# Performance work log

Hardware: AMD Instinct MI355X
Metric: run time of the kernel (lower is better)

The kernel has to match this reference:

```python
import jax, jax.numpy as jnp
import numpy as np

B, N, D, FF, L = 32, 1000, 128, 512, 6
EPS = 1e-5  # InstanceNorm1d default eps


def _inorm(x, g, b):
    # InstanceNorm1d on [B, d, N] == normalize over sequence dim N per channel (biased var)
    m = jnp.mean(x, axis=1, keepdims=True)
    v = jnp.var(x, axis=1, keepdims=True)
    return (x - m) / jnp.sqrt(v + EPS) * g + b


def setup_inputs() -> dict:
    key = jax.random.key(0)
    ks = jax.random.split(key, 10)
    s = 0.05
    data = jax.random.normal(ks[0], (B, N, 2), dtype=jnp.float32)
    # negative pairwise distances (module calls it negative_dist)
    dist = -jax.random.uniform(ks[1], (B, N, N), dtype=jnp.float32)
    log_scale = jnp.ones((1,), dtype=jnp.float32)
    We = jax.random.normal(ks[2], (D, 2), dtype=jnp.float32) * s
    be = jnp.zeros((D,), dtype=jnp.float32)
    Wq = jax.random.normal(ks[3], (L, D, D), dtype=jnp.float32) * s
    Wk = jax.random.normal(ks[4], (L, D, D), dtype=jnp.float32) * s
    Wv = jax.random.normal(ks[5], (L, D, D), dtype=jnp.float32) * s
    g1 = jnp.ones((L, D), dtype=jnp.float32)
    b1 = jnp.zeros((L, D), dtype=jnp.float32)
    W1 = jax.random.normal(ks[6], (L, FF, D), dtype=jnp.float32) * s
    bw1 = jnp.zeros((L, FF), dtype=jnp.float32)
    W2 = jax.random.normal(ks[7], (L, D, FF), dtype=jnp.float32) * s
    bw2 = jnp.zeros((L, D), dtype=jnp.float32)
    g2 = jnp.ones((L, D), dtype=jnp.float32)
    b2 = jnp.zeros((L, D), dtype=jnp.float32)
    alpha = jnp.ones((L,), dtype=jnp.float32)  # AFT_dist_alpha per layer
    return dict(data=data, dist=dist, log_scale=log_scale, We=We, be=be,
                Wq=Wq, Wk=Wk, Wv=Wv, g1=g1, b1=b1, W1=W1, bw1=bw1,
                W2=W2, bw2=bw2, g2=g2, b2=b2, alpha=alpha)


def reference(data, dist, log_scale, We, be, Wq, Wk, Wv, g1, b1, W1, bw1, W2, bw2, g2, b2, alpha):
    x = data @ We.T + be  # [B,N,D]
    for i in range(L):
        q = x @ Wq[i].T
        k = x @ Wk[i].T
        v = x @ Wv[i].T
        A = jnp.exp(log_scale[0] * alpha[i] * dist)  # [B,N,N]
        ek = jnp.exp(k)
        bias = jnp.einsum('bnm,bmd->bnd', A, ek * v)
        denom = jnp.einsum('bnm,bmd->bnd', A, ek)
        out = jax.nn.sigmoid(q) * (bias / denom)
        x1 = _inorm(x + out, g1[i], b1[i])
        h = jax.nn.relu(x1 @ W1[i].T + bw1[i]) @ W2[i].T + bw2[i]
        x = _inorm(x1 + h, g2[i], b2[i])
    return x
```

## Files before the change

### kernel.cpp

```cpp
#include <hip/hip_runtime.h>
#include <hip/hip_bf16.h>

typedef __attribute__((ext_vector_type(4))) float f32x4;
typedef __attribute__((ext_vector_type(8))) short bf16x8;
typedef __attribute__((ext_vector_type(4))) short s16x4;

#define LCOUNT 6

static __device__ __forceinline__ unsigned short f2b(float f){
  __hip_bfloat16 h = __float2bfloat16(f);
  return __builtin_bit_cast(unsigned short, h);
}
static __device__ __forceinline__ float b2f(unsigned short u){
  unsigned int x = ((unsigned int)u) << 16;
  return __builtin_bit_cast(float, x);
}
static __device__ __forceinline__ void gl16(const void* g, void* l){
  __builtin_amdgcn_global_load_lds(
      (const __attribute__((address_space(1))) void*)g,
      (__attribute__((address_space(3))) void*)l, 16, 0, 0);
}
static __device__ __forceinline__ f32x4 mfma16(bf16x8 a, bf16x8 b, f32x4 c){
  return __builtin_amdgcn_mfma_f32_16x16x32_bf16(a, b, c, 0, 0, 0);
}

__global__ void k_cvt5(const float* __restrict__ Wq, const float* __restrict__ Wk,
                       const float* __restrict__ Wv, const float* __restrict__ W1,
                       const float* __restrict__ W2,
                       unsigned short* __restrict__ wqb, unsigned short* __restrict__ wkb,
                       unsigned short* __restrict__ wvb, unsigned short* __restrict__ w1b,
                       unsigned short* __restrict__ w2b){
  int i = blockIdx.x*256 + threadIdx.x;
  if (i < 98304) wqb[i] = f2b(Wq[i]);
  else if (i < 196608) wkb[i-98304] = f2b(Wk[i-98304]);
  else if (i < 294912) wvb[i-196608] = f2b(Wv[i-196608]);
  else if (i < 688128) w1b[i-294912] = f2b(W1[i-294912]);
  else w2b[i-688128] = f2b(W2[i-688128]);
}

__global__ void k_cvtdist(const float* __restrict__ dist, unsigned short* __restrict__ db){
  int t = blockIdx.x*256 + threadIdx.x;
  int row = t >> 7, ch = t & 127;
  bf16x8 w;
  if (ch >= 125){
#pragma unroll
    for (int e=0;e<8;e++) w[e] = 0;
  } else {
    const float* p = dist + (size_t)row*1000 + ch*8;
    f32x4 a = *(const f32x4*)p;
    f32x4 b = *(const f32x4*)(p + 4);
#pragma unroll
    for (int e=0;e<4;e++){ w[e] = (short)f2b(a[e]); w[4+e] = (short)f2b(b[e]); }
  }
  *(bf16x8*)&db[(size_t)row*1024 + ch*8] = w;
}

__global__ void k_embed(const float* __restrict__ data, const float* __restrict__ We,
                        const float* __restrict__ be, float* __restrict__ x,
                        unsigned short* __restrict__ xb){
  int idx = blockIdx.x*256 + threadIdx.x;
  int d = idx & 127, bn = idx >> 7;
  float v = data[bn*2]*We[d*2] + data[bn*2+1]*We[d*2+1] + be[d];
  x[idx] = v; xb[idx] = f2b(v);
}

__global__ void k_scale(const float* __restrict__ part, int cnt,
                        const float* __restrict__ g, const float* __restrict__ beta,
                        float* __restrict__ na, float* __restrict__ nc){
  int b = blockIdx.x, d = threadIdx.x;
  float s1 = 0.f, s2 = 0.f;
  for (int c = 0; c < cnt; ++c){
    size_t pi = (((size_t)b*cnt + c)*128 + d)*2;
    s1 += part[pi]; s2 += part[pi+1];
  }
  float mean = s1 * 1e-3f;
  float var  = s2 * 1e-3f - mean*mean;
  float a = g[d] * rsqrtf(var + 1e-5f);
  na[b*128 + d] = a; nc[b*128 + d] = beta[d] - mean*a;
}

__global__ __launch_bounds__(256) void k_fapply(
  const float* __restrict__ x, const float* __restrict__ na,
  const float* __restrict__ nc, float* __restrict__ dout){
  int blk = blockIdx.x, tid = threadIdx.x;
  int b = blk / 125;
  size_t base = (size_t)blk*1024 + tid*4;
  int d0 = (tid*4) & 127;
  f32x4 v = *(const f32x4*)&x[base];
  f32x4 o;
#pragma unroll
  for (int e=0;e<4;e++) o[e] = v[e]*na[b*128 + d0 + e] + nc[b*128 + d0 + e];
  *(f32x4*)&dout[base] = o;
}

template<int NORM>
__global__ __launch_bounds__(256) void k_qkv(
  const unsigned short* __restrict__ xb, const float* __restrict__ x,
  const float* __restrict__ na2, const float* __restrict__ nc2,
  const unsigned short* __restrict__ Wqb, const unsigned short* __restrict__ Wkb,
  const unsigned short* __restrict__ Wvb,
  unsigned short* __restrict__ sigq, unsigned short* __restrict__ Zc)
{
  __shared__ unsigned short LA[2*2048];
  __shared__ unsigned short LB[2][4][256][8];
  __shared__ float sna[128], snc[128];
  int tid = threadIdx.x, wid = tid>>6, lane = tid&63;
  int l15 = lane&15, lg = lane>>4;
  int wm = wid>>1, wn = wid&1;
  int bt = blockIdx.x, b = bt>>4, t = bt&15;
  int kv = blockIdx.y;
  int lrow = t*64 + lane; if (lrow > 999) lrow = 999;
  size_t arow = (size_t)(b*1000 + lrow);

  if (NORM){
    if (tid < 128){ sna[tid] = na2[b*128 + tid]; snc[tid] = nc2[b*128 + tid]; }
    __syncthreads();
  }

  f32x4 zf = {0.f,0.f,0.f,0.f};
  f32x4 acc[2][4], acc2[2][4];
#pragma unroll
  for (int i=0;i<2;i++)
#pragma unroll
    for (int j=0;j<4;j++){ acc[i][j] = zf; acc2[i][j] = zf; }

  auto stage = [&](int kk, int buf){
    int k0 = kk*32;
    if (NORM){
      const float* p = x + arow*128 + k0 + wid*8;
      f32x4 v0 = *(const f32x4*)p;
      f32x4 v1 = *(const f32x4*)(p + 4);
      bf16x8 w;
#pragma unroll
      for (int e=0;e<4;e++){
        int k = k0 + wid*8;
        w[e]   = (short)f2b(v0[e]*sna[k+e]   + snc[k+e]);
        w[4+e] = (short)f2b(v1[e]*sna[k+4+e] + snc[k+4+e]);
      }
      *(bf16x8*)&LA[buf*2048 + wid*512 + lane*8] = w;
    } else {
      gl16(xb + arow*128 + k0 + wid*8, &LA[buf*2048 + wid*512]);
    }
    if (kv == 0){
#pragma unroll
      for (int t2=0;t2<2;++t2){
        int e = wid + t2*4, g2 = e>>1, nb = e&1;
        gl16(Wqb + (size_t)(nb*64+lane)*128 + k0 + g2*8, &LB[buf][g2][nb*64][0]);
      }
    } else {
#pragma unroll
      for (int t2=0;t2<4;++t2){
        int e = wid + t2*4, g2 = e&3, nb = e>>2;
        const unsigned short* src = (nb < 2)
          ? Wkb + (size_t)(nb*64+lane)*128 + k0 + g2*8
          : Wvb + (size_t)((nb-2)*64+lane)*128 + k0 + g2*8;
        gl16(src, &LB[buf][g2][nb*64][0]);
      }
    }
  };
  auto compute = [&](int buf){
    bf16x8 af[2];
#pragma unroll
    for (int i=0;i<2;i++){
      int row = wm*32 + i*16 + l15;
      af[i] = *(const bf16x8*)&LA[buf*2048 + lg*512 + row*8];
    }
#pragma unroll
    for (int j=0;j<4;j++){
      bf16x8 bq = *(const bf16x8*)&LB[buf][lg][wn*64 + j*16 + l15][0];
#pragma unroll
      for (int i=0;i<2;i++) acc[i][j] = mfma16(af[i], bq, acc[i][j]);
      if (kv){
        bf16x8 bv = *(const bf16x8*)&LB[buf][lg][128 + wn*64 + j*16 + l15][0];
#pragma unroll
        for (int i=0;i<2;i++) acc2[i][j] = mfma16(af[i], bv, acc2[i][j]);
      }
    }
  };

  stage(0, 0);
  __syncthreads();
  for (int kk = 0; kk < 4; ++kk){
    int buf = kk & 1;
    if (kk < 3) stage(kk+1, buf^1);
    compute(buf);
    __syncthreads();
  }

#pragma unroll
  for (int i=0;i<2;i++){
    int m4 = t*64 + wm*32 + i*16 + lg*4;
    if (m4 >= 1000) continue;
#pragma unroll
    for (int j=0;j<4;j++){
      int col = wn*64 + j*16 + l15;
      if (kv == 0){
#pragma unroll
        for (int r=0;r<4;r++)
          sigq[(size_t)(b*1000 + m4 + r)*128 + col] = f2b(1.f/(1.f + __expf(-acc[i][j][r])));
      } else {
        s16x4 pv, pk;
#pragma unroll
        for (int r=0;r<4;r++){
          float ek = __expf(acc[i][j][r]);
          pk[r] = (short)f2b(ek);
          pv[r] = (short)f2b(ek * acc2[i][j][r]);
        }
        size_t base = ((size_t)(b*128 + (m4>>3))*256 + col)*8 + ((m4>>2)&1)*4;
        *(s16x4*)&Zc[base] = pv;
        *(s16x4*)&Zc[base + 1024] = pk;
      }
    }
  }
}

template<int NORM, int USE16>
__global__ __launch_bounds__(256) void k_attn(
  const float* __restrict__ dist, const unsigned short* __restrict__ db16,
  const unsigned short* __restrict__ Zc, const unsigned short* __restrict__ sigq,
  float* __restrict__ x, float* __restrict__ partA,
  const float* __restrict__ na2, const float* __restrict__ nc2,
  const float* __restrict__ log_scale, const float* __restrict__ alpha, int layer)
{
  union SM {
    struct { unsigned short A[2][8][64][8]; unsigned short B[2][8][256][8]; } st;
    float den[64][128];
  };
  __shared__ SM sm;
  int tid = threadIdx.x, wid = tid>>6, lane = tid&63;
  int l15 = lane&15, lg = lane>>4;
  int bb = blockIdx.y, t = blockIdx.x, n0 = t*64;
  float sc = log_scale[0]*alpha[layer];
  const unsigned short* Zb = Zc + ((size_t)bb << 18);
  int an = n0 + lane; if (an > 999) an = 999;
  const size_t drow = (size_t)(bb*1000 + an);

  f32x4 zf = {0.f,0.f,0.f,0.f};
  f32x4 acc[4][4];
#pragma unroll
  for (int i=0;i<4;i++)
#pragma unroll
    for (int j=0;j<4;j++) acc[i][j] = zf;

  auto issueB = [&](int kk, int buf){
#pragma unroll
    for (int t2=0;t2<8;++t2){
      int e = wid + t2*4;
      int g2 = e >> 2, cb = e & 3;
      gl16(Zb + ((size_t)((kk*8 + g2)*256 + cb*64 + lane))*8, &sm.st.B[buf][g2][cb*64][0]);
    }
  };
  auto loadA2 = [&](int kk, float* v0, float* v1){
    int k0 = kk*64 + wid*8;
    int k1 = k0 + 32;
    if (USE16){
      bf16x8 r0 = *(const bf16x8*)(db16 + drow*1024 + k0);
      bf16x8 r1 = *(const bf16x8*)(db16 + drow*1024 + k1);
#pragma unroll
      for (int e=0;e<8;e++){ v0[e] = b2f((unsigned short)r0[e]); v1[e] = b2f((unsigned short)r1[e]); }
    } else {
      const float* dp = dist + drow*1000;
#pragma unroll
      for (int e=0;e<8;e++){
        int m0 = k0 + e; if (m0 > 999) m0 = 999;
        int m1 = k1 + e; if (m1 > 999) m1 = 999;
        v0[e] = dp[m0]; v1[e] = dp[m1];
      }
    }
  };
  auto expwrite2 = [&](const float* v0, const float* v1, int buf){
    bf16x8 w0, w1;
#pragma unroll
    for (int e=0;e<8;e++){
      w0[e] = (short)f2b(__expf(sc*v0[e]));
      w1[e] = (short)f2b(__expf(sc*v1[e]));
    }
    *(bf16x8*)&sm.st.A[buf][wid][lane][0]     = w0;
    *(bf16x8*)&sm.st.A[buf][wid+4][lane][0]   = w1;
  };
  auto compute = [&](int buf){
#pragma unroll
    for (int ks=0; ks<2; ++ks){
      bf16x8 af[4], bq[4];
#pragma unroll
      for (int i=0;i<4;i++) af[i] = *(const bf16x8*)&sm.st.A[buf][ks*4+lg][i*16 + l15][0];
#pragma unroll
      for (int j=0;j<4;j++) bq[j] = *(const bf16x8*)&sm.st.B[buf][ks*4+lg][wid*64 + j*16 + l15][0];
#pragma unroll
      for (int i=0;i<4;i++)
#pragma unroll
        for (int j=0;j<4;j++)
          acc[i][j] = mfma16(af[i], bq[j], acc[i][j]);
    }
  };

  float av0[8], av1[8];
  issueB(0, 0);
  loadA2(0, av0, av1);
  expwrite2(av0, av1, 0);
  __syncthreads();
  for (int kk = 0; kk < 16; ++kk){
    int buf = kk & 1;
    float nv0[8], nv1[8];
    if (kk < 15){ issueB(kk+1, buf^1); loadA2(kk+1, nv0, nv1); }
    compute(buf);
    if (kk < 15) expwrite2(nv0, nv1, buf^1);
    __syncthreads();
  }

  if (wid >= 2){
#pragma unroll
    for (int i=0;i<4;i++)
#pragma unroll
      for (int j=0;j<4;j++){
        int dcol = (wid-2)*64 + j*16 + l15;
#pragma unroll
        for (int r=0;r<4;r++)
          sm.den[i*16 + lg*4 + r][dcol] = acc[i][j][r];
      }
  }
  __syncthreads();
  if (wid < 2){
    float nav[4], ncv[4];
    if (NORM){
#pragma unroll
      for (int j=0;j<4;j++){
        int d = wid*64 + j*16 + l15;
        nav[j] = na2[bb*128 + d]; ncv[j] = nc2[bb*128 + d];
      }
    }
    float s1[4] = {0.f,0.f,0.f,0.f}, s2[4] = {0.f,0.f,0.f,0.f};
#pragma unroll
    for (int i=0;i<4;i++){
#pragma unroll
      for (int r=0;r<4;r++){
        int n = n0 + i*16 + lg*4 + r;
        if (n < 1000){
          size_t rowi = ((size_t)bb*1000 + n)*128;
#pragma unroll
          for (int j=0;j<4;j++){
            int d = wid*64 + j*16 + l15;
            float xv = x[rowi + d];
            if (NORM) xv = xv*nav[j] + ncv[j];
            float y = xv + b2f(sigq[rowi + d]) * acc[i][j][r] / sm.den[i*16 + lg*4 + r][d];
            x[rowi + d] = y;
            s1[j] += y; s2[j] += y*y;
          }
        }
      }
    }
#pragma unroll
    for (int j=0;j<4;j++){
      s1[j] += __shfl_xor(s1[j], 16); s2[j] += __shfl_xor(s2[j], 16);
      s1[j] += __shfl_xor(s1[j], 32); s2[j] += __shfl_xor(s2[j], 32);
    }
    if (lg == 0){
#pragma unroll
      for (int j=0;j<4;j++){
        int d = wid*64 + j*16 + l15;
        size_t pi = (((size_t)bb*16 + t)*128 + d)*2;
        partA[pi] = s1[j]; partA[pi+1] = s2[j];
      }
    }
  }
}

__global__ __launch_bounds__(512) void k_ff1(
  const float* __restrict__ x, const float* __restrict__ partA,
  const float* __restrict__ g1, const float* __restrict__ b1,
  const unsigned short* __restrict__ W1b, const float* __restrict__ bw1,
  float* __restrict__ x1, unsigned short* __restrict__ h1)
{
  __shared__ unsigned short LA[2][4][64][8];
  __shared__ unsigned short LB[2][4][512][8];
  __shared__ float sna[128], snc[128];
  int tid = threadIdx.x, wid = tid>>6, lane = tid&63;
  int l15 = lane&15, lg = lane>>4;
  int wm = wid>>2, wn = wid&3;
  int bt = blockIdx.x, b = bt>>4, t = bt&15;

  if (tid < 128){
    float s1 = 0.f, s2 = 0.f;
    for (int c = 0; c < 16; ++c){
      size_t pi = (((size_t)b*16 + c)*128 + tid)*2;
      s1 += partA[pi]; s2 += partA[pi+1];
    }
    float mean = s1 * 1e-3f;
    float var  = s2 * 1e-3f - mean*mean;
    float a = g1[tid] * rsqrtf(var + 1e-5f);
    sna[tid] = a; snc[tid] = b1[tid] - mean*a;
  }
  __syncthreads();

  f32x4 zf = {0.f,0.f,0.f,0.f};
  f32x4 acc[2][8];
#pragma unroll
  for (int i=0;i<2;i++)
#pragma unroll
    for (int j=0;j<8;j++) acc[i][j] = zf;

  auto stage = [&](int kk, int buf){
    int k0 = kk*32;
    if (tid < 256){
      int row = tid & 63, g2 = tid >> 6;
      int lr = t*64 + row;
      int rr = lr > 999 ? 999 : lr;
      const float* p = x + ((size_t)(b*1000 + rr))*128 + k0 + g2*8;
      f32x4 v0 = *(const f32x4*)p;
      f32x4 v1 = *(const f32x4*)(p + 4);
      f32x4 o0, o1;
      bf16x8 w;
#pragma unroll
      for (int e=0;e<4;e++){
        int k = k0 + g2*8;
        o0[e] = v0[e]*sna[k+e]   + snc[k+e];
        o1[e] = v1[e]*sna[k+4+e] + snc[k+4+e];
        w[e]   = (short)f2b(o0[e]);
        w[4+e] = (short)f2b(o1[e]);
      }
      *(bf16x8*)&LA[buf][g2][row][0] = w;
      if (lr < 1000){
        float* q = x1 + ((size_t)(b*1000 + lr))*128 + k0 + g2*8;
        *(f32x4*)q = o0; *(f32x4*)(q+4) = o1;
      }
    }
#pragma unroll
    for (int t2=0;t2<4;++t2){
      int e = wid*4 + t2;
      int g2 = e & 3, nb = e >> 2;
      gl16(W1b + (size_t)(nb*64 + lane)*128 + k0 + g2*8, &LB[buf][g2][nb*64][0]);
    }
  };
  auto compute = [&](int buf){
    bf16x8 af[2];
#pragma unroll
    for (int i=0;i<2;i++) af[i] = *(const bf16x8*)&LA[buf][lg][wm*32 + i*16 + l15][0];
#pragma unroll
    for (int j=0;j<8;j++){
      bf16x8 bq = *(const bf16x8*)&LB[buf][lg][wn*128 + j*16 + l15][0];
#pragma unroll
      for (int i=0;i<2;i++) acc[i][j] = mfma16(af[i], bq, acc[i][j]);
    }
  };

  stage(0, 0);
  __syncthreads();
  for (int kk = 0; kk < 4; ++kk){
    int buf = kk & 1;
    if (kk < 3) stage(kk+1, buf^1);
    compute(buf);
    __syncthreads();
  }

#pragma unroll
  for (int i=0;i<2;i++){
    int m4 = t*64 + wm*32 + i*16 + lg*4;
    if (m4 >= 1000) continue;
#pragma unroll
    for (int j=0;j<8;j++){
      int col = wn*128 + j*16 + l15;
      float bz = bw1[col];
#pragma unroll
      for (int r=0;r<4;r++){
        float v = acc[i][j][r] + bz;
        h1[(size_t)(b*1000 + m4 + r)*512 + col] = f2b(v > 0.f ? v : 0.f);
      }
    }
  }
}

__global__ __launch_bounds__(256) void k_ff2(
  const unsigned short* __restrict__ h1, const unsigned short* __restrict__ W2b,
  const float* __restrict__ bw2, const float* __restrict__ x1,
  float* __restrict__ x, float* __restrict__ partF)
{
  __shared__ unsigned short LA[2][8][64][8];
  __shared__ unsigned short LB[2][8][128][8];
  int tid = threadIdx.x, wid = tid>>6, lane = tid&63;
  int l15 = lane&15, lg = lane>>4;
  int wm = wid>>1, wn = wid&1;
  int bt = blockIdx.x, b = bt>>4, t = bt&15;
  int lrow = t*64 + lane; if (lrow > 999) lrow = 999;
  size_t arow = (size_t)(b*1000 + lrow);

  f32x4 zf = {0.f,0.f,0.f,0.f};
  f32x4 acc[2][4];
#pragma unroll
  for (int i=0;i<2;i++)
#pragma unroll
    for (int j=0;j<4;j++) acc[i][j] = zf;

  auto stage = [&](int kk, int buf){
    int k0 = kk*64;
#pragma unroll
    for (int t2=0;t2<2;++t2){
      int g2 = wid + t2*4;
      gl16(h1 + arow*512 + k0 + g2*8, &LA[buf][g2][0][0]);
    }
#pragma unroll
    for (int t2=0;t2<4;++t2){
      int e = wid*4 + t2;
      int g2 = e >> 1, nb = e & 1;
      gl16(W2b + (size_t)(nb*64 + lane)*512 + k0 + g2*8, &LB[buf][g2][nb*64][0]);
    }
  };
  auto compute = [&](int buf){
#pragma unroll
    for (int ks=0; ks<2; ++ks){
      bf16x8 af[2];
#pragma unroll
      for (int i=0;i<2;i++) af[i] = *(const bf16x8*)&LA[buf][ks*4+lg][wm*32 + i*16 + l15][0];
#pragma unroll
      for (int j=0;j<4;j++){
        bf16x8 bq = *(const bf16x8*)&LB[buf][ks*4+lg][wn*64 + j*16 + l15][0];
#pragma unroll
        for (int i=0;i<2;i++) acc[i][j] = mfma16(af[i], bq, acc[i][j]);
      }
    }
  };

  stage(0, 0);
  __syncthreads();
  for (int kk = 0; kk < 8; ++kk){
    int buf = kk & 1;
    if (kk < 7) stage(kk+1, buf^1);
    compute(buf);
    __syncthreads();
  }

  float s1[4] = {0.f,0.f,0.f,0.f}, s2[4] = {0.f,0.f,0.f,0.f};
#pragma unroll
  for (int i=0;i<2;i++){
    int m4 = t*64 + wm*32 + i*16 + lg*4;
    if (m4 >= 1000) continue;
#pragma unroll
    for (int j=0;j<4;j++){
      int col = wn*64 + j*16 + l15;
      float bz = bw2[col];
#pragma unroll
      for (int r=0;r<4;r++){
        size_t idx = (size_t)(b*1000 + m4 + r)*128 + col;
        float y = acc[i][j][r] + bz + x1[idx];
        x[idx] = y;
        s1[j] += y; s2[j] += y*y;
      }
    }
  }
#pragma unroll
  for (int j=0;j<4;j++){
    s1[j] += __shfl_xor(s1[j], 16); s2[j] += __shfl_xor(s2[j], 16);
    s1[j] += __shfl_xor(s1[j], 32); s2[j] += __shfl_xor(s2[j], 32);
  }
  if (lg == 0){
#pragma unroll
    for (int j=0;j<4;j++){
      int d = wn*64 + j*16 + l15;
      size_t pi = (((size_t)b*32 + t*2 + wm)*128 + d)*2;
      partF[pi] = s1[j]; partF[pi+1] = s2[j];
    }
  }
}

extern "C" void kernel_launch(void* const* d_in, const int* in_sizes, int n_in,
                              void* d_out, int out_size, void* d_ws, size_t ws_size,
                              hipStream_t stream) {
  const float* data = (const float*)d_in[0];
  const float* dist = (const float*)d_in[1];
  const float* log_scale = (const float*)d_in[2];
  const float* We = (const float*)d_in[3];
  const float* be = (const float*)d_in[4];
  const float* Wq = (const float*)d_in[5];
  const float* Wk = (const float*)d_in[6];
  const float* Wv = (const float*)d_in[7];
  const float* g1 = (const float*)d_in[8];
  const float* b1 = (const float*)d_in[9];
  const float* W1 = (const float*)d_in[10];
  const float* bw1 = (const float*)d_in[11];
  const float* W2 = (const float*)d_in[12];
  const float* bw2 = (const float*)d_in[13];
  const float* g2 = (const float*)d_in[14];
  const float* b2 = (const float*)d_in[15];
  const float* alpha = (const float*)d_in[16];
  float* dout = (float*)d_out;

  char* ws = (char*)d_ws;
  size_t off = 0;
  auto alloc = [&](size_t bytes) -> void* {
    void* p = ws + off; off += (bytes + 255) & ~(size_t)255; return p;
  };
  unsigned short* xb  = (unsigned short*)alloc(8192000);
  float* x            = (float*)alloc(16384000);
  unsigned short* sigq= (unsigned short*)alloc(8192000);
  unsigned short* Zc  = (unsigned short*)alloc(16777216);
  unsigned short* h1  = (unsigned short*)alloc(32768000);
  float* x1           = (float*)alloc(16384000);
  float* partA        = (float*)alloc(524288);
  float* partF        = (float*)alloc(1048576);
  float* na2          = (float*)alloc(16384);
  float* nc2          = (float*)alloc(16384);
  unsigned short* wqb = (unsigned short*)alloc(196608);
  unsigned short* wkb = (unsigned short*)alloc(196608);
  unsigned short* wvb = (unsigned short*)alloc(196608);
  unsigned short* w1b = (unsigned short*)alloc(786432);
  unsigned short* w2b = (unsigned short*)alloc(786432);
  if (off > ws_size) return;
  unsigned short* db16p = nullptr;
  if (ws_size >= off + 131072256) db16p = (unsigned short*)alloc(131072000);

  hipMemsetAsync(Zc, 0, 16777216, stream);
  k_cvt5<<<4224, 256, 0, stream>>>(Wq, Wk, Wv, W1, W2, wqb, wkb, wvb, w1b, w2b);
  if (db16p) k_cvtdist<<<16000, 256, 0, stream>>>(dist, db16p);
  k_embed<<<16000, 256, 0, stream>>>(data, We, be, x, xb);

  for (int i = 0; i < LCOUNT; ++i){
    if (i > 0)
      k_scale<<<32, 128, 0, stream>>>(partF, 32, g2 + (i-1)*128, b2 + (i-1)*128, na2, nc2);
    if (i == 0)
      k_qkv<0><<<dim3(512,2), 256, 0, stream>>>(xb, x, nullptr, nullptr,
                                                wqb + i*16384, wkb + i*16384, wvb + i*16384,
                                                sigq, Zc);
    else
      k_qkv<1><<<dim3(512,2), 256, 0, stream>>>(nullptr, x, na2, nc2,
                                                wqb + i*16384, wkb + i*16384, wvb + i*16384,
                                                sigq, Zc);
    if (i == 0){
      if (db16p) k_attn<0,1><<<dim3(16,32), 256, 0, stream>>>(dist, db16p, Zc, sigq, x, partA,
                                                              nullptr, nullptr, log_scale, alpha, i);
      else       k_attn<0,0><<<dim3(16,32), 256, 0, stream>>>(dist, nullptr, Zc, sigq, x, partA,
                                                              nullptr, nullptr, log_scale, alpha, i);
    } else {
      if (db16p) k_attn<1,1><<<dim3(16,32), 256, 0, stream>>>(dist, db16p, Zc, sigq, x, partA,
                                                              na2, nc2, log_scale, alpha, i);
      else       k_attn<1,0><<<dim3(16,32), 256, 0, stream>>>(dist, nullptr, Zc, sigq, x, partA,
                                                              na2, nc2, log_scale, alpha, i);
    }
    k_ff1<<<512, 512, 0, stream>>>(x, partA, g1 + i*128, b1 + i*128,
                                   w1b + i*65536, bw1 + i*512, x1, h1);
    k_ff2<<<512, 256, 0, stream>>>(h1, w2b + i*65536, bw2 + i*128, x1, x, partF);
  }
  k_scale<<<32, 128, 0, stream>>>(partF, 32, g2 + 5*128, b2 + 5*128, na2, nc2);
  k_fapply<<<4000, 256, 0, stream>>>(x, na2, nc2, dout);
}
```

Before: 836.6 us.

## Split attention kernel across two channel-column groups to double block count

The attention kernel now launches 32x32 blocks instead of 16x32. Each block handles 64 of the 128 output channels, for both the numerator and denominator halves, and the four waves are arranged 2x2 over rows and columns. This doubles the grid from 512 blocks to give the 256 compute units more blocks and improve occupancy. In exchange, every block recomputes exp(dist) for its A tile, so that exp work and the dist reads are duplicated. The per-row-half partial statistics layout grows to 32 slices, and the ff1 reduction is updated to match.

New measurement: 925.3 us. 1.11x slower.

```diff
diff --git a/kernel.cpp b/kernel.cpp
--- a/kernel.cpp
+++ b/kernel.cpp
@@ -223,31 +223,34 @@
   const float* __restrict__ log_scale, const float* __restrict__ alpha, int layer)
 {
   union SM {
-    struct { unsigned short A[2][8][64][8]; unsigned short B[2][8][256][8]; } st;
-    float den[64][128];
+    struct { unsigned short A[2][8][64][8]; unsigned short B[2][8][128][8]; } st;
+    float den[64][64];
   };
   __shared__ SM sm;
   int tid = threadIdx.x, wid = tid>>6, lane = tid&63;
   int l15 = lane&15, lg = lane>>4;
-  int bb = blockIdx.y, t = blockIdx.x, n0 = t*64;
+  int wm = wid>>1, wn = wid&1;
+  int bx = blockIdx.x, t = bx>>1, cg = bx&1;
+  int bb = blockIdx.y, n0 = t*64;
   float sc = log_scale[0]*alpha[layer];
   const unsigned short* Zb = Zc + ((size_t)bb << 18);
   int an = n0 + lane; if (an > 999) an = 999;
   const size_t drow = (size_t)(bb*1000 + an);
 
   f32x4 zf = {0.f,0.f,0.f,0.f};
-  f32x4 acc[4][4];
-#pragma unroll
-  for (int i=0;i<4;i++)
+  f32x4 acc[2][4];
+#pragma unroll
+  for (int i=0;i<2;i++)
 #pragma unroll
     for (int j=0;j<4;j++) acc[i][j] = zf;
 
   auto issueB = [&](int kk, int buf){
 #pragma unroll
-    for (int t2=0;t2<8;++t2){
-      int e = wid + t2*4;
-      int g2 = e >> 2, cb = e & 3;
-      gl16(Zb + ((size_t)((kk*8 + g2)*256 + cb*64 + lane))*8, &sm.st.B[buf][g2][cb*64][0]);
+    for (int t2=0;t2<4;++t2){
+      int e = wid*4 + t2;
+      int g2 = e >> 1, nb = e & 1;
+      int colb = nb ? (128 + cg*64) : (cg*64);
+      gl16(Zb + ((size_t)((kk*8 + g2)*256 + colb + lane))*8, &sm.st.B[buf][g2][nb*64][0]);
     }
   };
   auto loadA2 = [&](int kk, float* v0, float* v1){
@@ -275,19 +278,19 @@
       w0[e] = (short)f2b(__expf(sc*v0[e]));
       w1[e] = (short)f2b(__expf(sc*v1[e]));
     }
-    *(bf16x8*)&sm.st.A[buf][wid][lane][0]     = w0;
-    *(bf16x8*)&sm.st.A[buf][wid+4][lane][0]   = w1;
+    *(bf16x8*)&sm.st.A[buf][wid][lane][0]   = w0;
+    *(bf16x8*)&sm.st.A[buf][wid+4][lane][0] = w1;
   };
   auto compute = [&](int buf){
 #pragma unroll
     for (int ks=0; ks<2; ++ks){
-      bf16x8 af[4], bq[4];
-#pragma unroll
-      for (int i=0;i<4;i++) af[i] = *(const bf16x8*)&sm.st.A[buf][ks*4+lg][i*16 + l15][0];
-#pragma unroll
-      for (int j=0;j<4;j++) bq[j] = *(const bf16x8*)&sm.st.B[buf][ks*4+lg][wid*64 + j*16 + l15][0];
-#pragma unroll
-      for (int i=0;i<4;i++)
+      bf16x8 af[2], bq[4];
+#pragma unroll
+      for (int i=0;i<2;i++) af[i] = *(const bf16x8*)&sm.st.A[buf][ks*4+lg][wm*32 + i*16 + l15][0];
+#pragma unroll
+      for (int j=0;j<4;j++) bq[j] = *(const bf16x8*)&sm.st.B[buf][ks*4+lg][wn*64 + j*16 + l15][0];
+#pragma unroll
+      for (int i=0;i<2;i++)
 #pragma unroll
         for (int j=0;j<4;j++)
           acc[i][j] = mfma16(af[i], bq[j], acc[i][j]);
@@ -308,41 +311,40 @@
     __syncthreads();
   }
 
-  if (wid >= 2){
-#pragma unroll
-    for (int i=0;i<4;i++)
-#pragma unroll
-      for (int j=0;j<4;j++){
-        int dcol = (wid-2)*64 + j*16 + l15;
+  if (wn == 1){
+#pragma unroll
+    for (int i=0;i<2;i++)
+#pragma unroll
+      for (int j=0;j<4;j++)
 #pragma unroll
         for (int r=0;r<4;r++)
-          sm.den[i*16 + lg*4 + r][dcol] = acc[i][j][r];
-      }
+          sm.den[wm*32 + i*16 + lg*4 + r][j*16 + l15] = acc[i][j][r];
   }
   __syncthreads();
-  if (wid < 2){
+  if (wn == 0){
     float nav[4], ncv[4];
     if (NORM){
 #pragma unroll
       for (int j=0;j<4;j++){
-        int d = wid*64 + j*16 + l15;
+        int d = cg*64 + j*16 + l15;
         nav[j] = na2[bb*128 + d]; ncv[j] = nc2[bb*128 + d];
       }
     }
     float s1[4] = {0.f,0.f,0.f,0.f}, s2[4] = {0.f,0.f,0.f,0.f};
 #pragma unroll
-    for (int i=0;i<4;i++){
+    for (int i=0;i<2;i++){
 #pragma unroll
       for (int r=0;r<4;r++){
-        int n = n0 + i*16 + lg*4 + r;
+        int lr = wm*32 + i*16 + lg*4 + r;
+        int n = n0 + lr;
         if (n < 1000){
           size_t rowi = ((size_t)bb*1000 + n)*128;
 #pragma unroll
           for (int j=0;j<4;j++){
-            int d = wid*64 + j*16 + l15;
+            int d = cg*64 + j*16 + l15;
             float xv = x[rowi + d];
             if (NORM) xv = xv*nav[j] + ncv[j];
-            float y = xv + b2f(sigq[rowi + d]) * acc[i][j][r] / sm.den[i*16 + lg*4 + r][d];
+            float y = xv + b2f(sigq[rowi + d]) * acc[i][j][r] / sm.den[lr][j*16 + l15];
             x[rowi + d] = y;
             s1[j] += y; s2[j] += y*y;
           }
@@ -357,8 +359,8 @@
     if (lg == 0){
 #pragma unroll
       for (int j=0;j<4;j++){
-        int d = wid*64 + j*16 + l15;
-        size_t pi = (((size_t)bb*16 + t)*128 + d)*2;
+        int d = cg*64 + j*16 + l15;
+        size_t pi = (((size_t)bb*32 + t*2 + wm)*128 + d)*2;
         partA[pi] = s1[j]; partA[pi+1] = s2[j];
       }
     }
@@ -381,8 +383,8 @@
 
   if (tid < 128){
     float s1 = 0.f, s2 = 0.f;
-    for (int c = 0; c < 16; ++c){
-      size_t pi = (((size_t)b*16 + c)*128 + tid)*2;
+    for (int c = 0; c < 32; ++c){
+      size_t pi = (((size_t)b*32 + c)*128 + tid)*2;
       s1 += partA[pi]; s2 += partA[pi+1];
     }
     float mean = s1 * 1e-3f;
@@ -594,7 +596,7 @@
   unsigned short* Zc  = (unsigned short*)alloc(16777216);
   unsigned short* h1  = (unsigned short*)alloc(32768000);
   float* x1           = (float*)alloc(16384000);
-  float* partA        = (float*)alloc(524288);
+  float* partA        = (float*)alloc(1048576);
   float* partF        = (float*)alloc(1048576);
   float* na2          = (float*)alloc(16384);
   float* nc2          = (float*)alloc(16384);
@@ -624,14 +626,14 @@
                                                 wqb + i*16384, wkb + i*16384, wvb + i*16384,
                                                 sigq, Zc);
     if (i == 0){
-      if (db16p) k_attn<0,1><<<dim3(16,32), 256, 0, stream>>>(dist, db16p, Zc, sigq, x, partA,
+      if (db16p) k_attn<0,1><<<dim3(32,32), 256, 0, stream>>>(dist, db16p, Zc, sigq, x, partA,
                                                               nullptr, nullptr, log_scale, alpha, i);
-      else       k_attn<0,0><<<dim3(16,32), 256, 0, stream>>>(dist, nullptr, Zc, sigq, x, partA,
+      else       k_attn<0,0><<<dim3(32,32), 256, 0, stream>>>(dist, nullptr, Zc, sigq, x, partA,
                                                               nullptr, nullptr, log_scale, alpha, i);
     } else {
-      if (db16p) k_attn<1,1><<<dim3(16,32), 256, 0, stream>>>(dist, db16p, Zc, sigq, x, partA,
+      if (db16p) k_attn<1,1><<<dim3(32,32), 256, 0, stream>>>(dist, db16p, Zc, sigq, x, partA,
                                                               na2, nc2, log_scale, alpha, i);
-      else       k_attn<1,0><<<dim3(16,32), 256, 0, stream>>>(dist, nullptr, Zc, sigq, x, partA,
+      else       k_attn<1,0><<<dim3(32,32), 256, 0, stream>>>(dist, nullptr, Zc, sigq, x, partA,
                                                               na2, nc2, log_scale, alpha, i);
     }
     k_ff1<<<512, 512, 0, stream>>>(x, partA, g1 + i*128, b1 + i*128,
```

## Restructure attention kernel so each wave owns 16 rows with no LDS

Applied to the files above, without the earlier changes.

The attention kernel drops shared-memory staging and the block-wide split of numerator and denominator columns. Each wave now handles 16 query rows and computes both the bias and denominator accumulators (256 columns) directly, reading the exp(dist) A-fragments and Z B-fragments straight from global memory. Instance-norm partial sums are emitted per wave, so there are now 64 partials per batch, and the partial buffer and the reduction in k_ff1 are resized to match. This removes the __syncthreads barriers and LDS traffic. In exchange, B-fragment reuse across waves now has to come from L1/L2 rather than shared memory, and the kernel holds more accumulator registers.

Result: slower. 1.092 ms (+30.5%).

```diff
diff --git a/kernel.cpp b/kernel.cpp
--- a/kernel.cpp
+++ b/kernel.cpp
@@ -222,145 +222,92 @@
   const float* __restrict__ na2, const float* __restrict__ nc2,
   const float* __restrict__ log_scale, const float* __restrict__ alpha, int layer)
 {
-  union SM {
-    struct { unsigned short A[2][8][64][8]; unsigned short B[2][8][256][8]; } st;
-    float den[64][128];
-  };
-  __shared__ SM sm;
   int tid = threadIdx.x, wid = tid>>6, lane = tid&63;
   int l15 = lane&15, lg = lane>>4;
-  int bb = blockIdx.y, t = blockIdx.x, n0 = t*64;
+  int bb = blockIdx.y, t = blockIdx.x;
+  int n0 = t*64 + wid*16;
   float sc = log_scale[0]*alpha[layer];
   const unsigned short* Zb = Zc + ((size_t)bb << 18);
-  int an = n0 + lane; if (an > 999) an = 999;
+  int an = n0 + l15; if (an > 999) an = 999;
   const size_t drow = (size_t)(bb*1000 + an);
 
   f32x4 zf = {0.f,0.f,0.f,0.f};
-  f32x4 acc[4][4];
-#pragma unroll
-  for (int i=0;i<4;i++)
-#pragma unroll
-    for (int j=0;j<4;j++) acc[i][j] = zf;
-
-  auto issueB = [&](int kk, int buf){
-#pragma unroll
-    for (int t2=0;t2<8;++t2){
-      int e = wid + t2*4;
-      int g2 = e >> 2, cb = e & 3;
-      gl16(Zb + ((size_t)((kk*8 + g2)*256 + cb*64 + lane))*8, &sm.st.B[buf][g2][cb*64][0]);
-    }
-  };
-  auto loadA2 = [&](int kk, float* v0, float* v1){
-    int k0 = kk*64 + wid*8;
-    int k1 = k0 + 32;
+  f32x4 accB[8], accD[8];
+#pragma unroll
+  for (int j=0;j<8;j++){ accB[j] = zf; accD[j] = zf; }
+
+#pragma unroll 2
+  for (int kk = 0; kk < 32; ++kk){
+    int k0 = kk*32 + lg*8;
+    bf16x8 af;
     if (USE16){
-      bf16x8 r0 = *(const bf16x8*)(db16 + drow*1024 + k0);
-      bf16x8 r1 = *(const bf16x8*)(db16 + drow*1024 + k1);
-#pragma unroll
-      for (int e=0;e<8;e++){ v0[e] = b2f((unsigned short)r0[e]); v1[e] = b2f((unsigned short)r1[e]); }
+      bf16x8 ar = *(const bf16x8*)(db16 + drow*1024 + k0);
+#pragma unroll
+      for (int e=0;e<8;e++) af[e] = (short)f2b(__expf(sc*b2f((unsigned short)ar[e])));
     } else {
       const float* dp = dist + drow*1000;
-#pragma unroll
-      for (int e=0;e<8;e++){
-        int m0 = k0 + e; if (m0 > 999) m0 = 999;
-        int m1 = k1 + e; if (m1 > 999) m1 = 999;
-        v0[e] = dp[m0]; v1[e] = dp[m1];
-      }
-    }
-  };
-  auto expwrite2 = [&](const float* v0, const float* v1, int buf){
-    bf16x8 w0, w1;
-#pragma unroll
-    for (int e=0;e<8;e++){
-      w0[e] = (short)f2b(__expf(sc*v0[e]));
-      w1[e] = (short)f2b(__expf(sc*v1[e]));
-    }
-    *(bf16x8*)&sm.st.A[buf][wid][lane][0]     = w0;
-    *(bf16x8*)&sm.st.A[buf][wid+4][lane][0]   = w1;
-  };
-  auto compute = [&](int buf){
-#pragma unroll
-    for (int ks=0; ks<2; ++ks){
-      bf16x8 af[4], bq[4];
-#pragma unroll
-      for (int i=0;i<4;i++) af[i] = *(const bf16x8*)&sm.st.A[buf][ks*4+lg][i*16 + l15][0];
-#pragma unroll
-      for (int j=0;j<4;j++) bq[j] = *(const bf16x8*)&sm.st.B[buf][ks*4+lg][wid*64 + j*16 + l15][0];
-#pragma unroll
-      for (int i=0;i<4;i++)
-#pragma unroll
-        for (int j=0;j<4;j++)
-          acc[i][j] = mfma16(af[i], bq[j], acc[i][j]);
-    }
-  };
-
-  float av0[8], av1[8];
-  issueB(0, 0);
-  loadA2(0, av0, av1);
-  expwrite2(av0, av1, 0);
-  __syncthreads();
-  for (int kk = 0; kk < 16; ++kk){
-    int buf = kk & 1;
-    float nv0[8], nv1[8];
-    if (kk < 15){ issueB(kk+1, buf^1); loadA2(kk+1, nv0, nv1); }
-    compute(buf);
-    if (kk < 15) expwrite2(nv0, nv1, buf^1);
-    __syncthreads();
-  }
-
-  if (wid >= 2){
-#pragma unroll
-    for (int i=0;i<4;i++)
-#pragma unroll
-      for (int j=0;j<4;j++){
-        int dcol = (wid-2)*64 + j*16 + l15;
-#pragma unroll
-        for (int r=0;r<4;r++)
-          sm.den[i*16 + lg*4 + r][dcol] = acc[i][j][r];
-      }
-  }
-  __syncthreads();
-  if (wid < 2){
-    float nav[4], ncv[4];
-    if (NORM){
-#pragma unroll
-      for (int j=0;j<4;j++){
-        int d = wid*64 + j*16 + l15;
-        nav[j] = na2[bb*128 + d]; ncv[j] = nc2[bb*128 + d];
-      }
-    }
-    float s1[4] = {0.f,0.f,0.f,0.f}, s2[4] = {0.f,0.f,0.f,0.f};
-#pragma unroll
-    for (int i=0;i<4;i++){
-#pragma unroll
-      for (int r=0;r<4;r++){
-        int n = n0 + i*16 + lg*4 + r;
-        if (n < 1000){
-          size_t rowi = ((size_t)bb*1000 + n)*128;
-#pragma unroll
-          for (int j=0;j<4;j++){
-            int d = wid*64 + j*16 + l15;
-            float xv = x[rowi + d];
-            if (NORM) xv = xv*nav[j] + ncv[j];
-            float y = xv + b2f(sigq[rowi + d]) * acc[i][j][r] / sm.den[i*16 + lg*4 + r][d];
-            x[rowi + d] = y;
-            s1[j] += y; s2[j] += y*y;
-          }
+      if (k0 + 8 <= 1000){
+        f32x4 a0 = *(const f32x4*)(dp + k0);
+        f32x4 a1 = *(const f32x4*)(dp + k0 + 4);
+#pragma unroll
+        for (int e=0;e<4;e++){
+          af[e]   = (short)f2b(__expf(sc*a0[e]));
+          af[4+e] = (short)f2b(__expf(sc*a1[e]));
         }
-      }
-    }
-#pragma unroll
-    for (int j=0;j<4;j++){
-      s1[j] += __shfl_xor(s1[j], 16); s2[j] += __shfl_xor(s2[j], 16);
-      s1[j] += __shfl_xor(s1[j], 32); s2[j] += __shfl_xor(s2[j], 32);
-    }
-    if (lg == 0){
-#pragma unroll
-      for (int j=0;j<4;j++){
-        int d = wid*64 + j*16 + l15;
-        size_t pi = (((size_t)bb*16 + t)*128 + d)*2;
-        partA[pi] = s1[j]; partA[pi+1] = s2[j];
-      }
+      } else {
+#pragma unroll
+        for (int e=0;e<8;e++){
+          int m = k0 + e; if (m > 999) m = 999;
+          af[e] = (short)f2b(__expf(sc*dp[m]));
+        }
+      }
+    }
+    const unsigned short* zk = Zb + ((size_t)(kk*4 + lg))*2048;
+#pragma unroll
+    for (int j=0;j<8;j++){
+      bf16x8 bqB = *(const bf16x8*)(zk + (j*16 + l15)*8);
+      bf16x8 bqD = *(const bf16x8*)(zk + (128 + j*16 + l15)*8);
+      accB[j] = mfma16(af, bqB, accB[j]);
+      accD[j] = mfma16(af, bqD, accD[j]);
+    }
+  }
+
+  float nav[8], ncv[8];
+  if (NORM){
+#pragma unroll
+    for (int j=0;j<8;j++){
+      int d = j*16 + l15;
+      nav[j] = na2[bb*128 + d]; ncv[j] = nc2[bb*128 + d];
+    }
+  }
+  float s1[8] = {0,0,0,0,0,0,0,0}, s2[8] = {0,0,0,0,0,0,0,0};
+#pragma unroll
+  for (int r=0;r<4;r++){
+    int n = n0 + lg*4 + r;
+    if (n < 1000){
+      size_t rowi = ((size_t)bb*1000 + n)*128;
+#pragma unroll
+      for (int j=0;j<8;j++){
+        int d = j*16 + l15;
+        float xv = x[rowi + d];
+        if (NORM) xv = xv*nav[j] + ncv[j];
+        float y = xv + b2f(sigq[rowi + d]) * accB[j][r] / accD[j][r];
+        x[rowi + d] = y;
+        s1[j] += y; s2[j] += y*y;
+      }
+    }
+  }
+#pragma unroll
+  for (int j=0;j<8;j++){
+    s1[j] += __shfl_xor(s1[j], 16); s2[j] += __shfl_xor(s2[j], 16);
+    s1[j] += __shfl_xor(s1[j], 32); s2[j] += __shfl_xor(s2[j], 32);
+  }
+  if (lg == 0){
+#pragma unroll
+    for (int j=0;j<8;j++){
+      int d = j*16 + l15;
+      size_t pi = (((size_t)bb*64 + t*4 + wid)*128 + d)*2;
+      partA[pi] = s1[j]; partA[pi+1] = s2[j];
     }
   }
 }
@@ -381,8 +328,8 @@
 
   if (tid < 128){
     float s1 = 0.f, s2 = 0.f;
-    for (int c = 0; c < 16; ++c){
-      size_t pi = (((size_t)b*16 + c)*128 + tid)*2;
+    for (int c = 0; c < 64; ++c){
+      size_t pi = (((size_t)b*64 + c)*128 + tid)*2;
       s1 += partA[pi]; s2 += partA[pi+1];
     }
     float mean = s1 * 1e-3f;
@@ -594,7 +541,7 @@
   unsigned short* Zc  = (unsigned short*)alloc(16777216);
   unsigned short* h1  = (unsigned short*)alloc(32768000);
   float* x1           = (float*)alloc(16384000);
-  float* partA        = (float*)alloc(524288);
+  float* partA        = (float*)alloc(2097152);
   float* partF        = (float*)alloc(1048576);
   float* na2          = (float*)alloc(16384);
   float* nc2          = (float*)alloc(16384);
```
